# Kernel tuning notes

Measured on AMD Instinct MI355X. Metric: run time of the kernel, lower is better.

Reference implementation:

```python
import jax, jax.numpy as jnp
import numpy as np

N_NODES = 500000
N_EDGES = 5000000


def _sage_conv(x, edge_index, Wl, bl, Wr):
    # PyG SAGEConv (aggr='mean', root_weight=True):
    #   out = lin_l(mean_{j in N(i)} x_j) + lin_r(x_i)
    # edge_index[0] = source, edge_index[1] = target
    src, dst = edge_index[0], edge_index[1]
    n = x.shape[0]
    msg = x[src]  # [E, F] gather
    agg = jax.ops.segment_sum(msg, dst, num_segments=n)  # [N, F]
    deg = jax.ops.segment_sum(jnp.ones((src.shape[0],), x.dtype), dst, num_segments=n)
    agg = agg / jnp.maximum(deg, 1.0)[:, None]  # mean aggregation
    return agg @ Wl.T + bl + x @ Wr.T


def setup_inputs() -> dict:
    key = jax.random.key(0)
    k1, k2, k3, k4, k5, k6 = jax.random.split(key, 6)
    x = jax.random.normal(k1, (N_NODES, 2), dtype=jnp.float32)
    edge_index = jax.random.randint(k2, (2, N_EDGES), 0, N_NODES, dtype=jnp.int64)
    # conv1: SAGEConv(2, 16); conv2: SAGEConv(16, 1)
    s1 = 1.0 / np.sqrt(2.0)
    s2 = 1.0 / np.sqrt(16.0)
    W1l = jax.random.uniform(k3, (16, 2), jnp.float32, -s1, s1)
    W1r = jax.random.uniform(k4, (16, 2), jnp.float32, -s1, s1)
    b1 = jnp.zeros((16,), jnp.float32)
    W2l = jax.random.uniform(k5, (1, 16), jnp.float32, -s2, s2)
    W2r = jax.random.uniform(k6, (1, 16), jnp.float32, -s2, s2)
    b2 = jnp.zeros((1,), jnp.float32)
    return {"x": x, "edge_index": edge_index,
            "W1l": W1l, "b1": b1, "W1r": W1r,
            "W2l": W2l, "b2": b2, "W2r": W2r}


def reference(x, edge_index, W1l, b1, W1r, W2l, b2, W2r):
    h = jax.nn.relu(_sage_conv(x, edge_index, W1l, b1, W1r))  # [N, 16]
    h = _sage_conv(h, edge_index, W2l, b2, W2r)               # [N, 1]
    return jax.nn.sigmoid(h).squeeze(-1)                      # [N]
```

## Files before the change

### kernel.cpp

```cpp
#include <hip/hip_runtime.h>


static constexpr int ABLOCK = 512;
static constexpr int PBLOCK = 1024;
static constexpr int KITER  = 5;
static constexpr int CHUNK  = PBLOCK * 4 * KITER;
static constexpr int BUCKET_BITS = 10;
static constexpr int BUCKET_NODES = 1 << BUCKET_BITS;
static constexpr int MAXNB = 512;
static constexpr int CAP = 16384;
static constexpr int CSTRIDE = 16;

static constexpr float S1 = 2048.0f;
static constexpr float IS1 = 1.0f / 2048.0f;
static constexpr long long B1 = 8LL * 2048LL;
static constexpr float S2 = 16384.0f;
static constexpr float IS2 = 1.0f / 16384.0f;

__global__ __launch_bounds__(256) void k_pre(
    const float* __restrict__ x, unsigned* __restrict__ qx,
    unsigned* __restrict__ cursor, int N, int NB)
{
    int i = blockIdx.x * 256 + threadIdx.x;
    if (i < NB) cursor[(size_t)i * CSTRIDE] = (unsigned)i * (unsigned)CAP;
    if (i >= N) return;
    float2 xv = *reinterpret_cast<const float2*>(x + 2 * (size_t)i);
    float f0 = fminf(fmaxf((xv.x + 8.0f) * S1, 0.0f), 65535.0f);
    float f1 = fminf(fmaxf((xv.y + 8.0f) * S1, 0.0f), 65535.0f);
    unsigned q0 = (unsigned)__float2int_rn(f0);
    unsigned q1 = (unsigned)__float2int_rn(f1);
    qx[i] = (q0 << 16) | q1;
}

__global__ __launch_bounds__(PBLOCK) void k_part(
    const int* __restrict__ src, const int* __restrict__ dst,
    unsigned* __restrict__ cursor, unsigned* __restrict__ entries,
    int E, int NB)
{
    __shared__ unsigned sorted[CHUNK];
    __shared__ unsigned hist[MAXNB];
    __shared__ unsigned loc[MAXNB];
    __shared__ unsigned base[MAXNB];
    const int tid = threadIdx.x;
    const int e0 = (int)blockIdx.x * CHUNK;
    const int e1 = min(e0 + CHUNK, E);
    const int4* dst4 = reinterpret_cast<const int4*>(dst + e0);
    const int4* src4 = reinterpret_cast<const int4*>(src + e0);

    int4 dR[KITER], sR[KITER];
#pragma unroll
    for (int k = 0; k < KITER; ++k) {
        int g = tid + k * PBLOCK;
        int e = e0 + 4 * g;
        if (e + 3 < e1) {
            dR[k] = dst4[g];
            sR[k] = src4[g];
        } else {
            dR[k] = make_int4(-1, -1, -1, -1);
            sR[k] = make_int4(0, 0, 0, 0);
#pragma unroll
            for (int j = 0; j < 4; ++j) {
                if (e + j < e1) {
                    (&dR[k].x)[j] = dst[e + j];
                    (&sR[k].x)[j] = src[e + j];
                }
            }
        }
    }

    for (int b = tid; b < MAXNB; b += PBLOCK) hist[b] = 0;
    __syncthreads();

    #define HIST1(dv) { unsigned du_ = (unsigned)(dv); \
        if (du_ != 0xFFFFFFFFu) atomicAdd(&hist[du_ >> BUCKET_BITS], 1u); }
#pragma unroll
    for (int k = 0; k < KITER; ++k) {
        HIST1(dR[k].x) HIST1(dR[k].y) HIST1(dR[k].z) HIST1(dR[k].w)
    }
    #undef HIST1
    __syncthreads();

    if (tid < NB) loc[tid] = hist[tid];
    __syncthreads();
    for (int off = 1; off < NB; off <<= 1) {
        unsigned v = 0;
        if (tid < NB && tid >= off) v = loc[tid - off];
        __syncthreads();
        if (tid < NB) loc[tid] += v;
        __syncthreads();
    }
    if (tid < NB) loc[tid] -= hist[tid];

    if (tid < NB) {
        int b = tid + (int)(blockIdx.x % (unsigned)NB);
        if (b >= NB) b -= NB;
        base[b] = atomicAdd(&cursor[(size_t)b * CSTRIDE], hist[b]);
    }
    __syncthreads();
    for (int b = tid; b < MAXNB; b += PBLOCK) hist[b] = 0;
    __syncthreads();

    #define SCAT1(dv, sv) { unsigned du_ = (unsigned)(dv); \
        if (du_ != 0xFFFFFFFFu) { \
            unsigned bk_ = du_ >> BUCKET_BITS; \
            unsigned r_ = atomicAdd(&hist[bk_], 1u); \
            sorted[loc[bk_] + r_] = ((unsigned)(sv) << BUCKET_BITS) | (du_ & (BUCKET_NODES - 1)); } }
#pragma unroll
    for (int k = 0; k < KITER; ++k) {
        SCAT1(dR[k].x, sR[k].x) SCAT1(dR[k].y, sR[k].y)
        SCAT1(dR[k].z, sR[k].z) SCAT1(dR[k].w, sR[k].w)
    }
    #undef SCAT1
    __syncthreads();

    const int wave = tid >> 6, lane = tid & 63;
    const int nw = PBLOCK >> 6;
    const int off = (int)(blockIdx.x % (unsigned)NB);
    for (int j = wave; j < NB; j += nw) {
        int b = j + off;
        if (b >= NB) b -= NB;
        unsigned cnt = hist[b];
        if (cnt == 0) continue;
        unsigned lo = loc[b], ba = base[b];
        unsigned lim = (unsigned)(b + 1) * (unsigned)CAP;
        if (ba >= lim) continue;
        cnt = min(cnt, lim - ba);
        for (unsigned i = lane; i < cnt; i += 64)
            entries[ba + i] = sorted[lo + i];
    }
}

#define PK(q) ((1ULL << 56) | ((unsigned long long)((q) >> 16) << 28) \
               | (unsigned long long)((q) & 0xFFFFu))

__global__ __launch_bounds__(ABLOCK) void k_agg1(
    const unsigned* __restrict__ entries, const unsigned* __restrict__ cursor,
    const unsigned* __restrict__ qx, const float* __restrict__ x,
    const float* __restrict__ W1l, const float* __restrict__ b1,
    const float* __restrict__ W1r, const float* __restrict__ W2l,
    const float* __restrict__ W2r, const float* __restrict__ b2,
    unsigned* __restrict__ sq, float* __restrict__ t0a, float* __restrict__ ga,
    int N)
{
    __shared__ unsigned long long qs[BUCKET_NODES];
    int bk = blockIdx.x;
    for (int i = threadIdx.x; i < BUCKET_NODES; i += ABLOCK) qs[i] = 0ULL;
    __syncthreads();

    unsigned start = (unsigned)bk * (unsigned)CAP;
    unsigned end = min(cursor[(size_t)bk * CSTRIDE], start + (unsigned)CAP);
    unsigned n = end - start;
    unsigned n8 = n >> 3;
    const uint4* e4 = reinterpret_cast<const uint4*>(entries + start);

    for (unsigned t = threadIdx.x; t < n8; t += ABLOCK) {
        uint4 a = e4[2 * t];
        uint4 b = e4[2 * t + 1];
        unsigned g0 = qx[a.x >> BUCKET_BITS];
        unsigned g1 = qx[a.y >> BUCKET_BITS];
        unsigned g2 = qx[a.z >> BUCKET_BITS];
        unsigned g3 = qx[a.w >> BUCKET_BITS];
        unsigned g4 = qx[b.x >> BUCKET_BITS];
        unsigned g5 = qx[b.y >> BUCKET_BITS];
        unsigned g6 = qx[b.z >> BUCKET_BITS];
        unsigned g7 = qx[b.w >> BUCKET_BITS];
        atomicAdd(&qs[a.x & (BUCKET_NODES - 1)], PK(g0));
        atomicAdd(&qs[a.y & (BUCKET_NODES - 1)], PK(g1));
        atomicAdd(&qs[a.z & (BUCKET_NODES - 1)], PK(g2));
        atomicAdd(&qs[a.w & (BUCKET_NODES - 1)], PK(g3));
        atomicAdd(&qs[b.x & (BUCKET_NODES - 1)], PK(g4));
        atomicAdd(&qs[b.y & (BUCKET_NODES - 1)], PK(g5));
        atomicAdd(&qs[b.z & (BUCKET_NODES - 1)], PK(g6));
        atomicAdd(&qs[b.w & (BUCKET_NODES - 1)], PK(g7));
    }
    for (unsigned t = start + (n8 << 3) + threadIdx.x; t < end; t += ABLOCK) {
        unsigned en = entries[t];
        unsigned g = qx[en >> BUCKET_BITS];
        atomicAdd(&qs[en & (BUCKET_NODES - 1)], PK(g));
    }
    __syncthreads();

    int nodebase = bk << BUCKET_BITS;
    for (int il = threadIdx.x; il < BUCKET_NODES; il += ABLOCK) {
        int i = nodebase + il;
        if (i >= N) continue;
        unsigned long long v = qs[il];
        int deg = (int)(v >> 56);
        long long q0 = (long long)((v >> 28) & 0xFFFFFFFULL);
        long long q1 = (long long)(v & 0xFFFFFFFULL);
        long long bias = (long long)deg * B1;
        float inv = 1.0f / (float)max(deg, 1);
        float m0 = (float)(q0 - bias) * IS1 * inv;
        float m1 = (float)(q1 - bias) * IS1 * inv;
        float2 xv = *reinterpret_cast<const float2*>(x + 2 * (size_t)i);
        float s = 0.0f, t0 = b2[0];
#pragma unroll
        for (int o = 0; o < 16; ++o) {
            float h = m0 * W1l[2 * o] + m1 * W1l[2 * o + 1] + b1[o]
                    + xv.x * W1r[2 * o] + xv.y * W1r[2 * o + 1];
            h = fmaxf(h, 0.0f);
            s  += h * W2l[o];
            t0 += h * W2r[o];
        }
        sq[i]  = (unsigned)__float2int_rn((s + 128.0f) * S2);
        t0a[i] = t0 - (deg > 0 ? 128.0f : 0.0f);
        ga[i]  = IS2 * inv;
    }
}

__global__ __launch_bounds__(ABLOCK) void k_agg2(
    const unsigned* __restrict__ entries, const unsigned* __restrict__ cursor,
    const unsigned* __restrict__ sq,
    const float* __restrict__ t0a, const float* __restrict__ ga,
    float* __restrict__ out, int N)
{
    __shared__ unsigned sbin[BUCKET_NODES];
    int bk = blockIdx.x;
    for (int i = threadIdx.x; i < BUCKET_NODES; i += ABLOCK) sbin[i] = 0;
    __syncthreads();

    unsigned start = (unsigned)bk * (unsigned)CAP;
    unsigned end = min(cursor[(size_t)bk * CSTRIDE], start + (unsigned)CAP);
    unsigned n = end - start;
    unsigned n8 = n >> 3;
    const uint4* e4 = reinterpret_cast<const uint4*>(entries + start);

    for (unsigned t = threadIdx.x; t < n8; t += ABLOCK) {
        uint4 a = e4[2 * t];
        uint4 b = e4[2 * t + 1];
        unsigned v0 = sq[a.x >> BUCKET_BITS];
        unsigned v1 = sq[a.y >> BUCKET_BITS];
        unsigned v2 = sq[a.z >> BUCKET_BITS];
        unsigned v3 = sq[a.w >> BUCKET_BITS];
        unsigned v4 = sq[b.x >> BUCKET_BITS];
        unsigned v5 = sq[b.y >> BUCKET_BITS];
        unsigned v6 = sq[b.z >> BUCKET_BITS];
        unsigned v7 = sq[b.w >> BUCKET_BITS];
        atomicAdd(&sbin[a.x & (BUCKET_NODES - 1)], v0);
        atomicAdd(&sbin[a.y & (BUCKET_NODES - 1)], v1);
        atomicAdd(&sbin[a.z & (BUCKET_NODES - 1)], v2);
        atomicAdd(&sbin[a.w & (BUCKET_NODES - 1)], v3);
        atomicAdd(&sbin[b.x & (BUCKET_NODES - 1)], v4);
        atomicAdd(&sbin[b.y & (BUCKET_NODES - 1)], v5);
        atomicAdd(&sbin[b.z & (BUCKET_NODES - 1)], v6);
        atomicAdd(&sbin[b.w & (BUCKET_NODES - 1)], v7);
    }
    for (unsigned t = start + (n8 << 3) + threadIdx.x; t < end; t += ABLOCK) {
        unsigned en = entries[t];
        atomicAdd(&sbin[en & (BUCKET_NODES - 1)], sq[en >> BUCKET_BITS]);
    }
    __syncthreads();

    int nodebase = bk << BUCKET_BITS;
    for (int il = threadIdx.x; il < BUCKET_NODES; il += ABLOCK) {
        int i = nodebase + il;
        if (i >= N) continue;
        float t = (float)(int)sbin[il] * ga[i] + t0a[i];
        out[i] = 1.0f / (1.0f + expf(-t));
    }
}

__global__ __launch_bounds__(256) void k_scatter1_fb(
    const int* __restrict__ src, const int* __restrict__ dst,
    const float* __restrict__ x, float* __restrict__ agg1, float* __restrict__ deg, int E)
{
    int stride = gridDim.x * blockDim.x;
    for (int e = blockIdx.x * blockDim.x + threadIdx.x; e < E; e += stride) {
        int s = src[e], d = dst[e];
        float2 xv = *reinterpret_cast<const float2*>(x + 2 * (size_t)s);
        unsafeAtomicAdd(&agg1[2 * (size_t)d + 0], xv.x);
        unsafeAtomicAdd(&agg1[2 * (size_t)d + 1], xv.y);
        unsafeAtomicAdd(&deg[d], 1.0f);
    }
}
__global__ __launch_bounds__(256) void k_node1_fb(
    const float* __restrict__ x, const float* __restrict__ agg1, const float* __restrict__ deg,
    const float* __restrict__ W1l, const float* __restrict__ b1,
    const float* __restrict__ W1r, const float* __restrict__ W2l,
    float* __restrict__ sval, int N)
{
    int i = blockIdx.x * blockDim.x + threadIdx.x;
    if (i >= N) return;
    float inv = 1.0f / fmaxf(deg[i], 1.0f);
    float2 a = *reinterpret_cast<const float2*>(agg1 + 2 * (size_t)i);
    float m0 = a.x * inv, m1 = a.y * inv;
    float2 xv = *reinterpret_cast<const float2*>(x + 2 * (size_t)i);
    float s = 0.0f;
#pragma unroll
    for (int o = 0; o < 16; ++o) {
        float h = m0 * W1l[2 * o] + m1 * W1l[2 * o + 1] + b1[o]
                + xv.x * W1r[2 * o] + xv.y * W1r[2 * o + 1];
        s += fmaxf(h, 0.0f) * W2l[o];
    }
    sval[i] = s;
}
__global__ __launch_bounds__(256) void k_scatter2_fb(
    const int* __restrict__ src, const int* __restrict__ dst,
    const float* __restrict__ sval, float* __restrict__ agg_s, int E)
{
    int stride = gridDim.x * blockDim.x;
    for (int e = blockIdx.x * blockDim.x + threadIdx.x; e < E; e += stride)
        unsafeAtomicAdd(&agg_s[dst[e]], sval[src[e]]);
}
__global__ __launch_bounds__(256) void k_node2_fb(
    const float* __restrict__ x, const float* __restrict__ agg1, const float* __restrict__ deg,
    const float* __restrict__ agg_s,
    const float* __restrict__ W1l, const float* __restrict__ b1,
    const float* __restrict__ W1r, const float* __restrict__ W2r, const float* __restrict__ b2,
    float* __restrict__ out, int N)
{
    int i = blockIdx.x * blockDim.x + threadIdx.x;
    if (i >= N) return;
    float inv = 1.0f / fmaxf(deg[i], 1.0f);
    float2 a = *reinterpret_cast<const float2*>(agg1 + 2 * (size_t)i);
    float m0 = a.x * inv, m1 = a.y * inv;
    float2 xv = *reinterpret_cast<const float2*>(x + 2 * (size_t)i);
    float t = agg_s[i] * inv + b2[0];
#pragma unroll
    for (int o = 0; o < 16; ++o) {
        float h = m0 * W1l[2 * o] + m1 * W1l[2 * o + 1] + b1[o]
                + xv.x * W1r[2 * o] + xv.y * W1r[2 * o + 1];
        t += fmaxf(h, 0.0f) * W2r[o];
    }
    out[i] = 1.0f / (1.0f + expf(-t));
}

extern "C" void kernel_launch(void* const* d_in, const int* in_sizes, int n_in,
                              void* d_out, int out_size, void* d_ws, size_t ws_size,
                              hipStream_t stream) {
    const float* x   = (const float*)d_in[0];
    const int*   ei  = (const int*)d_in[1];
    const float* W1l = (const float*)d_in[2];
    const float* b1  = (const float*)d_in[3];
    const float* W1r = (const float*)d_in[4];
    const float* W2l = (const float*)d_in[5];
    const float* b2  = (const float*)d_in[6];
    const float* W2r = (const float*)d_in[7];

    const int N = in_sizes[0] / 2;
    const int E = in_sizes[1] / 2;
    const int* src = ei;
    const int* dst = ei + (size_t)E;
    float* out = (float*)d_out;

    const int NB = (N + BUCKET_NODES - 1) >> BUCKET_BITS;
    const int pblocks = (E + CHUNK - 1) / CHUNK;

    size_t needed = (size_t)MAXNB * CSTRIDE * 4 + (size_t)NB * CAP * 4 + 4 * (size_t)N * 4;
    if (NB <= MAXNB && NB <= PBLOCK && ws_size >= needed) {
        unsigned* cursor  = (unsigned*)d_ws;
        unsigned* entries = cursor + (size_t)MAXNB * CSTRIDE;
        unsigned* sq      = entries + (size_t)NB * CAP;
        float*    t0a     = (float*)(sq + N);
        float*    ga      = t0a + N;
        unsigned* qx      = (unsigned*)(ga + N);

        k_pre<<<(N + 255) / 256, 256, 0, stream>>>(x, qx, cursor, N, NB);
        k_part<<<pblocks, PBLOCK, 0, stream>>>(src, dst, cursor, entries, E, NB);
        k_agg1<<<NB, ABLOCK, 0, stream>>>(entries, cursor, qx, x, W1l, b1, W1r,
                                          W2l, W2r, b2, sq, t0a, ga, N);
        k_agg2<<<NB, ABLOCK, 0, stream>>>(entries, cursor, sq, t0a, ga, out, N);
    } else {
        float* agg1  = (float*)d_ws;
        float* deg   = agg1 + 2 * (size_t)N;
        float* agg_s = deg + (size_t)N;
        float* sval  = agg_s + (size_t)N;
        hipMemsetAsync(d_ws, 0, 4 * (size_t)N * sizeof(float), stream);
        const int eblocks = 2048, nblocks = (N + 255) / 256;
        k_scatter1_fb<<<eblocks, 256, 0, stream>>>(src, dst, x, agg1, deg, E);
        k_node1_fb<<<nblocks, 256, 0, stream>>>(x, agg1, deg, W1l, b1, W1r, W2l, sval, N);
        k_scatter2_fb<<<eblocks, 256, 0, stream>>>(src, dst, sval, agg_s, E);
        k_node2_fb<<<nblocks, 256, 0, stream>>>(x, agg1, deg, agg_s, W1l, b1, W1r, W2r, b2, out, N);
    }
}
```

Before: 90.02 us.

## Split bucket queues into per-group segments and compact second-layer gather data

The partition kernel now spreads each bucket's append cursor over eight group sub-queues keyed by block index. This is meant to reduce global atomic contention on one cursor per bucket. Each aggregation wave then consumes its own segment. The block prefix scan is rewritten with wave shuffles instead of a log-step shared-memory loop. The layer-2 scalar is quantized to 16-bit to shrink the random gather, and the per-node terms are packed into one float2. Quantization drops from scale 16384 to 256, which loses precision. Each group segment has a fixed capacity of 2048 entries and silently drops overflow if the distribution is uneven.

```diff
diff --git a/kernel.cpp b/kernel.cpp
--- a/kernel.cpp
+++ b/kernel.cpp
@@ -8,21 +8,22 @@
 static constexpr int BUCKET_BITS = 10;
 static constexpr int BUCKET_NODES = 1 << BUCKET_BITS;
 static constexpr int MAXNB = 512;
-static constexpr int CAP = 16384;
+static constexpr int NGRP = 8;
+static constexpr int GCAP = 2048;
 static constexpr int CSTRIDE = 16;
 
 static constexpr float S1 = 2048.0f;
 static constexpr float IS1 = 1.0f / 2048.0f;
 static constexpr long long B1 = 8LL * 2048LL;
-static constexpr float S2 = 16384.0f;
-static constexpr float IS2 = 1.0f / 16384.0f;
+static constexpr float S2 = 256.0f;
+static constexpr float IS2 = 1.0f / 256.0f;
 
 __global__ __launch_bounds__(256) void k_pre(
     const float* __restrict__ x, unsigned* __restrict__ qx,
-    unsigned* __restrict__ cursor, int N, int NB)
+    unsigned* __restrict__ cursor, int N, int NBG)
 {
     int i = blockIdx.x * 256 + threadIdx.x;
-    if (i < NB) cursor[(size_t)i * CSTRIDE] = (unsigned)i * (unsigned)CAP;
+    if (i < NBG) cursor[(size_t)i * CSTRIDE] = (unsigned)i * (unsigned)GCAP;
     if (i >= N) return;
     float2 xv = *reinterpret_cast<const float2*>(x + 2 * (size_t)i);
     float f0 = fminf(fmaxf((xv.x + 8.0f) * S1, 0.0f), 65535.0f);
@@ -41,7 +42,9 @@
     __shared__ unsigned hist[MAXNB];
     __shared__ unsigned loc[MAXNB];
     __shared__ unsigned base[MAXNB];
+    __shared__ unsigned wsum[8];
     const int tid = threadIdx.x;
+    const unsigned g = blockIdx.x & (NGRP - 1);
     const int e0 = (int)blockIdx.x * CHUNK;
     const int e1 = min(e0 + CHUNK, E);
     const int4* dst4 = reinterpret_cast<const int4*>(dst + e0);
@@ -50,11 +53,11 @@
     int4 dR[KITER], sR[KITER];
 #pragma unroll
     for (int k = 0; k < KITER; ++k) {
-        int g = tid + k * PBLOCK;
-        int e = e0 + 4 * g;
+        int gi = tid + k * PBLOCK;
+        int e = e0 + 4 * gi;
         if (e + 3 < e1) {
-            dR[k] = dst4[g];
-            sR[k] = src4[g];
+            dR[k] = dst4[gi];
+            sR[k] = src4[gi];
         } else {
             dR[k] = make_int4(-1, -1, -1, -1);
             sR[k] = make_int4(0, 0, 0, 0);
@@ -80,21 +83,33 @@
     #undef HIST1
     __syncthreads();
 
-    if (tid < NB) loc[tid] = hist[tid];
-    __syncthreads();
-    for (int off = 1; off < NB; off <<= 1) {
-        unsigned v = 0;
-        if (tid < NB && tid >= off) v = loc[tid - off];
+    {
+        unsigned lane6 = (unsigned)tid & 63u, wv = (unsigned)tid >> 6;
+        unsigned hv = (tid < NB) ? hist[tid] : 0u;
+        if (tid < 512) {
+            unsigned v = hv;
+#pragma unroll
+            for (int off = 1; off < 64; off <<= 1) {
+                unsigned u = __shfl_up(v, off);
+                if (lane6 >= (unsigned)off) v += u;
+            }
+            if (lane6 == 63) wsum[wv] = v;
+            if (tid < NB) loc[tid] = v - hv;
+        }
         __syncthreads();
-        if (tid < NB) loc[tid] += v;
+        if (tid == 0) {
+            unsigned acc = 0;
+#pragma unroll
+            for (int k = 0; k < 8; ++k) { unsigned t2 = wsum[k]; wsum[k] = acc; acc += t2; }
+        }
         __syncthreads();
-    }
-    if (tid < NB) loc[tid] -= hist[tid];
+        if (tid < NB) loc[tid] += wsum[wv];
+    }
 
     if (tid < NB) {
         int b = tid + (int)(blockIdx.x % (unsigned)NB);
         if (b >= NB) b -= NB;
-        base[b] = atomicAdd(&cursor[(size_t)b * CSTRIDE], hist[b]);
+        base[b] = atomicAdd(&cursor[((size_t)b * NGRP + g) * CSTRIDE], hist[b]);
     }
     __syncthreads();
     for (int b = tid; b < MAXNB; b += PBLOCK) hist[b] = 0;
@@ -122,7 +137,7 @@
         unsigned cnt = hist[b];
         if (cnt == 0) continue;
         unsigned lo = loc[b], ba = base[b];
-        unsigned lim = (unsigned)(b + 1) * (unsigned)CAP;
+        unsigned lim = ((unsigned)b * NGRP + g + 1u) * (unsigned)GCAP;
         if (ba >= lim) continue;
         cnt = min(cnt, lim - ba);
         for (unsigned i = lane; i < cnt; i += 64)
@@ -139,7 +154,7 @@
     const float* __restrict__ W1l, const float* __restrict__ b1,
     const float* __restrict__ W1r, const float* __restrict__ W2l,
     const float* __restrict__ W2r, const float* __restrict__ b2,
-    unsigned* __restrict__ sq, float* __restrict__ t0a, float* __restrict__ ga,
+    unsigned short* __restrict__ sq, float2* __restrict__ tg,
     int N)
 {
     __shared__ unsigned long long qs[BUCKET_NODES];
@@ -147,36 +162,40 @@
     for (int i = threadIdx.x; i < BUCKET_NODES; i += ABLOCK) qs[i] = 0ULL;
     __syncthreads();
 
-    unsigned start = (unsigned)bk * (unsigned)CAP;
-    unsigned end = min(cursor[(size_t)bk * CSTRIDE], start + (unsigned)CAP);
-    unsigned n = end - start;
-    unsigned n8 = n >> 3;
-    const uint4* e4 = reinterpret_cast<const uint4*>(entries + start);
-
-    for (unsigned t = threadIdx.x; t < n8; t += ABLOCK) {
-        uint4 a = e4[2 * t];
-        uint4 b = e4[2 * t + 1];
-        unsigned g0 = qx[a.x >> BUCKET_BITS];
-        unsigned g1 = qx[a.y >> BUCKET_BITS];
-        unsigned g2 = qx[a.z >> BUCKET_BITS];
-        unsigned g3 = qx[a.w >> BUCKET_BITS];
-        unsigned g4 = qx[b.x >> BUCKET_BITS];
-        unsigned g5 = qx[b.y >> BUCKET_BITS];
-        unsigned g6 = qx[b.z >> BUCKET_BITS];
-        unsigned g7 = qx[b.w >> BUCKET_BITS];
-        atomicAdd(&qs[a.x & (BUCKET_NODES - 1)], PK(g0));
-        atomicAdd(&qs[a.y & (BUCKET_NODES - 1)], PK(g1));
-        atomicAdd(&qs[a.z & (BUCKET_NODES - 1)], PK(g2));
-        atomicAdd(&qs[a.w & (BUCKET_NODES - 1)], PK(g3));
-        atomicAdd(&qs[b.x & (BUCKET_NODES - 1)], PK(g4));
-        atomicAdd(&qs[b.y & (BUCKET_NODES - 1)], PK(g5));
-        atomicAdd(&qs[b.z & (BUCKET_NODES - 1)], PK(g6));
-        atomicAdd(&qs[b.w & (BUCKET_NODES - 1)], PK(g7));
-    }
-    for (unsigned t = start + (n8 << 3) + threadIdx.x; t < end; t += ABLOCK) {
-        unsigned en = entries[t];
-        unsigned g = qx[en >> BUCKET_BITS];
-        atomicAdd(&qs[en & (BUCKET_NODES - 1)], PK(g));
+    {
+        const unsigned wv = (unsigned)threadIdx.x >> 6;
+        const unsigned lane = (unsigned)threadIdx.x & 63u;
+        const unsigned seg = (unsigned)bk * NGRP + wv;
+        const unsigned base0 = seg * (unsigned)GCAP;
+        unsigned end = min(cursor[(size_t)seg * CSTRIDE], base0 + (unsigned)GCAP);
+        unsigned len = end - base0;
+        unsigned t = 0;
+        for (; t + 512 <= len; t += 512) {
+            const uint4* p = reinterpret_cast<const uint4*>(entries + base0 + t + (lane << 3));
+            uint4 a = p[0];
+            uint4 b = p[1];
+            unsigned g0 = qx[a.x >> BUCKET_BITS];
+            unsigned g1 = qx[a.y >> BUCKET_BITS];
+            unsigned g2 = qx[a.z >> BUCKET_BITS];
+            unsigned g3 = qx[a.w >> BUCKET_BITS];
+            unsigned g4 = qx[b.x >> BUCKET_BITS];
+            unsigned g5 = qx[b.y >> BUCKET_BITS];
+            unsigned g6 = qx[b.z >> BUCKET_BITS];
+            unsigned g7 = qx[b.w >> BUCKET_BITS];
+            atomicAdd(&qs[a.x & (BUCKET_NODES - 1)], PK(g0));
+            atomicAdd(&qs[a.y & (BUCKET_NODES - 1)], PK(g1));
+            atomicAdd(&qs[a.z & (BUCKET_NODES - 1)], PK(g2));
+            atomicAdd(&qs[a.w & (BUCKET_NODES - 1)], PK(g3));
+            atomicAdd(&qs[b.x & (BUCKET_NODES - 1)], PK(g4));
+            atomicAdd(&qs[b.y & (BUCKET_NODES - 1)], PK(g5));
+            atomicAdd(&qs[b.z & (BUCKET_NODES - 1)], PK(g6));
+            atomicAdd(&qs[b.w & (BUCKET_NODES - 1)], PK(g7));
+        }
+        for (unsigned u = t + lane; u < len; u += 64) {
+            unsigned en = entries[base0 + u];
+            unsigned gq = qx[en >> BUCKET_BITS];
+            atomicAdd(&qs[en & (BUCKET_NODES - 1)], PK(gq));
+        }
     }
     __syncthreads();
 
@@ -202,16 +221,16 @@
             s  += h * W2l[o];
             t0 += h * W2r[o];
         }
-        sq[i]  = (unsigned)__float2int_rn((s + 128.0f) * S2);
-        t0a[i] = t0 - (deg > 0 ? 128.0f : 0.0f);
-        ga[i]  = IS2 * inv;
+        float fq = fminf(fmaxf((s + 128.0f) * S2, 0.0f), 65535.0f);
+        sq[i] = (unsigned short)__float2int_rn(fq);
+        tg[i] = make_float2(IS2 * inv, t0 - (deg > 0 ? 128.0f : 0.0f));
     }
 }
 
 __global__ __launch_bounds__(ABLOCK) void k_agg2(
     const unsigned* __restrict__ entries, const unsigned* __restrict__ cursor,
-    const unsigned* __restrict__ sq,
-    const float* __restrict__ t0a, const float* __restrict__ ga,
+    const unsigned short* __restrict__ sq,
+    const float2* __restrict__ tg,
     float* __restrict__ out, int N)
 {
     __shared__ unsigned sbin[BUCKET_NODES];
@@ -219,35 +238,39 @@
     for (int i = threadIdx.x; i < BUCKET_NODES; i += ABLOCK) sbin[i] = 0;
     __syncthreads();
 
-    unsigned start = (unsigned)bk * (unsigned)CAP;
-    unsigned end = min(cursor[(size_t)bk * CSTRIDE], start + (unsigned)CAP);
-    unsigned n = end - start;
-    unsigned n8 = n >> 3;
-    const uint4* e4 = reinterpret_cast<const uint4*>(entries + start);
-
-    for (unsigned t = threadIdx.x; t < n8; t += ABLOCK) {
-        uint4 a = e4[2 * t];
-        uint4 b = e4[2 * t + 1];
-        unsigned v0 = sq[a.x >> BUCKET_BITS];
-        unsigned v1 = sq[a.y >> BUCKET_BITS];
-        unsigned v2 = sq[a.z >> BUCKET_BITS];
-        unsigned v3 = sq[a.w >> BUCKET_BITS];
-        unsigned v4 = sq[b.x >> BUCKET_BITS];
-        unsigned v5 = sq[b.y >> BUCKET_BITS];
-        unsigned v6 = sq[b.z >> BUCKET_BITS];
-        unsigned v7 = sq[b.w >> BUCKET_BITS];
-        atomicAdd(&sbin[a.x & (BUCKET_NODES - 1)], v0);
-        atomicAdd(&sbin[a.y & (BUCKET_NODES - 1)], v1);
-        atomicAdd(&sbin[a.z & (BUCKET_NODES - 1)], v2);
-        atomicAdd(&sbin[a.w & (BUCKET_NODES - 1)], v3);
-        atomicAdd(&sbin[b.x & (BUCKET_NODES - 1)], v4);
-        atomicAdd(&sbin[b.y & (BUCKET_NODES - 1)], v5);
-        atomicAdd(&sbin[b.z & (BUCKET_NODES - 1)], v6);
-        atomicAdd(&sbin[b.w & (BUCKET_NODES - 1)], v7);
-    }
-    for (unsigned t = start + (n8 << 3) + threadIdx.x; t < end; t += ABLOCK) {
-        unsigned en = entries[t];
-        atomicAdd(&sbin[en & (BUCKET_NODES - 1)], sq[en >> BUCKET_BITS]);
+    {
+        const unsigned wv = (unsigned)threadIdx.x >> 6;
+        const unsigned lane = (unsigned)threadIdx.x & 63u;
+        const unsigned seg = (unsigned)bk * NGRP + wv;
+        const unsigned base0 = seg * (unsigned)GCAP;
+        unsigned end = min(cursor[(size_t)seg * CSTRIDE], base0 + (unsigned)GCAP);
+        unsigned len = end - base0;
+        unsigned t = 0;
+        for (; t + 512 <= len; t += 512) {
+            const uint4* p = reinterpret_cast<const uint4*>(entries + base0 + t + (lane << 3));
+            uint4 a = p[0];
+            uint4 b = p[1];
+            unsigned v0 = sq[a.x >> BUCKET_BITS];
+            unsigned v1 = sq[a.y >> BUCKET_BITS];
+            unsigned v2 = sq[a.z >> BUCKET_BITS];
+            unsigned v3 = sq[a.w >> BUCKET_BITS];
+            unsigned v4 = sq[b.x >> BUCKET_BITS];
+            unsigned v5 = sq[b.y >> BUCKET_BITS];
+            unsigned v6 = sq[b.z >> BUCKET_BITS];
+            unsigned v7 = sq[b.w >> BUCKET_BITS];
+            atomicAdd(&sbin[a.x & (BUCKET_NODES - 1)], v0);
+            atomicAdd(&sbin[a.y & (BUCKET_NODES - 1)], v1);
+            atomicAdd(&sbin[a.z & (BUCKET_NODES - 1)], v2);
+            atomicAdd(&sbin[a.w & (BUCKET_NODES - 1)], v3);
+            atomicAdd(&sbin[b.x & (BUCKET_NODES - 1)], v4);
+            atomicAdd(&sbin[b.y & (BUCKET_NODES - 1)], v5);
+            atomicAdd(&sbin[b.z & (BUCKET_NODES - 1)], v6);
+            atomicAdd(&sbin[b.w & (BUCKET_NODES - 1)], v7);
+        }
+        for (unsigned u = t + lane; u < len; u += 64) {
+            unsigned en = entries[base0 + u];
+            atomicAdd(&sbin[en & (BUCKET_NODES - 1)], (unsigned)sq[en >> BUCKET_BITS]);
+        }
     }
     __syncthreads();
 
@@ -255,7 +278,8 @@
     for (int il = threadIdx.x; il < BUCKET_NODES; il += ABLOCK) {
         int i = nodebase + il;
         if (i >= N) continue;
-        float t = (float)(int)sbin[il] * ga[i] + t0a[i];
+        float2 tgv = tg[i];
+        float t = (float)(int)sbin[il] * tgv.x + tgv.y;
         out[i] = 1.0f / (1.0f + expf(-t));
     }
 }
@@ -344,22 +368,25 @@
     float* out = (float*)d_out;
 
     const int NB = (N + BUCKET_NODES - 1) >> BUCKET_BITS;
+    const int NBG = NB * NGRP;
     const int pblocks = (E + CHUNK - 1) / CHUNK;
 
-    size_t needed = (size_t)MAXNB * CSTRIDE * 4 + (size_t)NB * CAP * 4 + 4 * (size_t)N * 4;
+    size_t needed = (size_t)MAXNB * NGRP * CSTRIDE * 4
+                  + (size_t)NBG * GCAP * 4
+                  + ((size_t)N * 2 + 3) / 4 * 4
+                  + (size_t)N * 8 + (size_t)N * 4 + 256;
     if (NB <= MAXNB && NB <= PBLOCK && ws_size >= needed) {
-        unsigned* cursor  = (unsigned*)d_ws;
-        unsigned* entries = cursor + (size_t)MAXNB * CSTRIDE;
-        unsigned* sq      = entries + (size_t)NB * CAP;
-        float*    t0a     = (float*)(sq + N);
-        float*    ga      = t0a + N;
-        unsigned* qx      = (unsigned*)(ga + N);
-
-        k_pre<<<(N + 255) / 256, 256, 0, stream>>>(x, qx, cursor, N, NB);
+        unsigned* cursor   = (unsigned*)d_ws;
+        unsigned* entries  = cursor + (size_t)MAXNB * NGRP * CSTRIDE;
+        unsigned short* sq = (unsigned short*)(entries + (size_t)NBG * GCAP);
+        float2*   tg       = (float2*)((char*)sq + (((size_t)N * 2 + 7) & ~7ull));
+        unsigned* qx       = (unsigned*)(tg + N);
+
+        k_pre<<<(N + 255) / 256, 256, 0, stream>>>(x, qx, cursor, N, NBG);
         k_part<<<pblocks, PBLOCK, 0, stream>>>(src, dst, cursor, entries, E, NB);
         k_agg1<<<NB, ABLOCK, 0, stream>>>(entries, cursor, qx, x, W1l, b1, W1r,
-                                          W2l, W2r, b2, sq, t0a, ga, N);
-        k_agg2<<<NB, ABLOCK, 0, stream>>>(entries, cursor, sq, t0a, ga, out, N);
+                                          W2l, W2r, b2, sq, tg, N);
+        k_agg2<<<NB, ABLOCK, 0, stream>>>(entries, cursor, sq, tg, out, N);
     } else {
         float* agg1  = (float*)d_ws;
         float* deg   = agg1 + 2 * (size_t)N;
```

After: 91.74 us. No clear change (+1.9%).
